# Kernel tuning notes

Hardware: AMD Instinct MI355X
Metric: run time of the kernel (lower is better)

Reference implementation:

```python
import jax, jax.numpy as jnp
import numpy as np
from jax import lax

B, T, D, H = 4, 2048, 1024, 8
DK = D // H        # head qk dim (expand_k=1.0) = 128
DV = 2 * D // H    # head v dim (expand_v=2.0) = 256
C = 64             # retention chunk size


def setup_inputs() -> dict:
    key = jax.random.key(0)
    ks = jax.random.split(key, 7)
    s = 0.02
    return {
        "x": jax.random.normal(ks[0], (B, T, D), jnp.float32),
        "Wq": jax.random.normal(ks[1], (D, H * DK), jnp.float32) * s,
        "Wk": jax.random.normal(ks[2], (D, H * DK), jnp.float32) * s,
        "Wv": jax.random.normal(ks[3], (D, H * DV), jnp.float32) * s,
        "Wg": jax.random.normal(ks[4], (D, H * DV), jnp.float32) * s,
        "Wo": jax.random.normal(ks[5], (H * DV, D), jnp.float32) * s,
        "norm_w": jnp.ones((DV,), jnp.float32),
    }


def _rope(x):
    # x: [B,T,H,DK]; GPT-NeoX style (non-interleaved) rotary, base 10000
    half = DK // 2
    inv = 1.0 / (10000.0 ** (jnp.arange(0, DK, 2, dtype=jnp.float32) / DK))
    f = jnp.arange(T, dtype=jnp.float32)[:, None] * inv[None, :]  # [T, half]
    cos = jnp.cos(f)[None, :, None, :]
    sin = jnp.sin(f)[None, :, None, :]
    x1, x2 = x[..., :half], x[..., half:]
    return jnp.concatenate([x1 * cos - x2 * sin, x2 * cos + x1 * sin], axis=-1)


def _retention(q, k, v):
    # chunked decay-gated linear attention (RetNet retention)
    # q,k: [B,T,H,DK], v: [B,T,H,DV]; recurrence S_t = g*S_{t-1} + k_t^T v_t, o_t = q_t S_t
    N = T // C
    gamma = 1.0 - 2.0 ** (-5.0 - jnp.arange(H, dtype=jnp.float32))  # [H] per-head decay
    i = jnp.arange(C, dtype=jnp.float32)
    expo = i[:, None] - i[None, :]                                   # [C,C]
    M = jnp.where(expo >= 0, gamma[:, None, None] ** expo[None], 0.0)  # [H,C,C] intra-chunk decay mask
    dec_q = gamma[:, None] ** (i + 1.0)        # [H,C] decay of state seen by q_i
    dec_k = gamma[:, None] ** (C - 1.0 - i)    # [H,C] decay of k_j into end-of-chunk state
    gC = gamma ** C

    def to_chunks(t):
        return t.reshape(B, N, C, H, -1).transpose(1, 0, 3, 2, 4)  # [N,B,H,C,d]

    qs, kcs, vcs = to_chunks(q), to_chunks(k), to_chunks(v)

    def step(S, inp):
        qc, kc, vc = inp  # [B,H,C,DK],[B,H,C,DK],[B,H,C,DV]
        attn = jnp.einsum('bhid,bhjd->bhij', qc, kc) * M[None]
        o_intra = jnp.einsum('bhij,bhje->bhie', attn, vc)
        o_inter = jnp.einsum('bhid,bhde->bhie', qc, S) * dec_q[None, :, :, None]
        kv = jnp.einsum('bhjd,bhje->bhde', kc * dec_k[None, :, :, None], vc)
        S_new = gC[None, :, None, None] * S + kv
        return S_new, o_intra + o_inter

    S0 = jnp.zeros((B, H, DK, DV), q.dtype)
    _, os_ = lax.scan(step, S0, (qs, kcs, vcs))  # os_: [N,B,H,C,DV]
    return os_.transpose(1, 0, 3, 2, 4).reshape(B, T, H, DV)


def reference(x, Wq, Wk, Wv, Wg, Wo, norm_w):
    q = (x @ Wq).reshape(B, T, H, DK)
    k = (x @ Wk).reshape(B, T, H, DK)
    v = (x @ Wv).reshape(B, T, H, DV)
    g = (x @ Wg).reshape(B, T, H, DV)
    q, k = _rope(q), _rope(k)
    q = q * (DK ** -0.5)
    o = _retention(q, k, v)
    # fused per-head RMSNorm + swish output gate (FusedRMSNormSwishGate)
    rms = jnp.sqrt(jnp.mean(o * o, axis=-1, keepdims=True) + 1e-5)
    o = (o / rms) * norm_w
    o = o * g * jax.nn.sigmoid(g)
    return o.reshape(B, T, H * DV) @ Wo
```

## Files before the change

kernel.cpp:

```cpp
#include <hip/hip_runtime.h>
#include <hip/hip_bf16.h>
#include <cstdint>
#include <cstddef>

using f32x4 = __attribute__((ext_vector_type(4))) float;
using s16x8 = __attribute__((ext_vector_type(8))) short;
using s16x4 = __attribute__((ext_vector_type(4))) short;

#define DEVINL __device__ __forceinline__

static constexpr int T_LEN  = 2048;
static constexpr int MROWS  = 8192;
static constexpr int NCHUNK = 32;

DEVINL float bf2f(short s){
  unsigned u = ((unsigned)(unsigned short)s) << 16;
  return __builtin_bit_cast(float, u);
}
DEVINL short f2bf(float f){
  unsigned u = __builtin_bit_cast(unsigned, f);
  u = (u + 0x7fffu + ((u >> 16) & 1u)) >> 16;
  return (short)(unsigned short)u;
}

#define GLOAD16(gp, lp) \
  __builtin_amdgcn_global_load_lds((__attribute__((address_space(1))) void*)(gp), \
                                   (__attribute__((address_space(3))) void*)(lp), 16, 0, 0)

#define MFMA16(a, b, c) __builtin_amdgcn_mfma_f32_16x16x32_bf16((a), (b), (c), 0, 0, 0)
#define SBAR()  __builtin_amdgcn_sched_barrier(0)
#define WAITLGKM(n) asm volatile("s_waitcnt lgkmcnt(" #n ")" ::: "memory")
#define WAITVM(n)   asm volatile("s_waitcnt vmcnt(" #n ")" ::: "memory")

__global__ __launch_bounds__(256) void cvt_f32_bf16(const float* __restrict__ in,
                                                    short* __restrict__ out, int n4){
  int i = blockIdx.x * 256 + threadIdx.x;
  if (i >= n4) return;
  float4 v = ((const float4*)in)[i];
  short4 o;
  o.x = f2bf(v.x); o.y = f2bf(v.y); o.z = f2bf(v.z); o.w = f2bf(v.w);
  ((short4*)out)[i] = o;
}

__global__ __launch_bounds__(256) void tr_w(const float* __restrict__ in,
                                            short* __restrict__ out, int R, int C){
  __shared__ float tile[32][33];
  int c0 = blockIdx.x * 32, r0 = blockIdx.y * 32;
  int tx = threadIdx.x, ty = threadIdx.y;
  #pragma unroll
  for (int i = 0; i < 4; ++i){
    int r = ty + i * 8;
    tile[r][tx] = in[(size_t)(r0 + r) * C + c0 + tx];
  }
  __syncthreads();
  #pragma unroll
  for (int i = 0; i < 4; ++i){
    int c = ty + i * 8;
    out[(size_t)(c0 + c) * R + r0 + tx] = f2bf(tile[tx][c]);
  }
}

__global__ __launch_bounds__(256) void tr_w4(const float* __restrict__ Wq,
                                             const float* __restrict__ Wk,
                                             const float* __restrict__ Wv,
                                             const float* __restrict__ Wg,
                                             short* __restrict__ WT){
  __shared__ float tile[32][33];
  int bx = blockIdx.x;
  const float* src; int C; size_t off; int cb;
  if (bx < 32)       { src = Wq; C = 1024; off = 0;                       cb = bx; }
  else if (bx < 64)  { src = Wk; C = 1024; off = (size_t)1024 * 1024;     cb = bx - 32; }
  else if (bx < 128) { src = Wg; C = 2048; off = (size_t)2048 * 1024;     cb = bx - 64; }
  else               { src = Wv; C = 2048; off = (size_t)4096 * 1024;     cb = bx - 128; }
  int c0 = cb * 32, r0 = blockIdx.y * 32;
  int tx = threadIdx.x, ty = threadIdx.y;
  #pragma unroll
  for (int i = 0; i < 4; ++i){
    int r = ty + i * 8;
    tile[r][tx] = src[(size_t)(r0 + r) * C + c0 + tx];
  }
  __syncthreads();
  #pragma unroll
  for (int i = 0; i < 4; ++i){
    int c = ty + i * 8;
    WT[off + (size_t)(c0 + c) * 1024 + r0 + tx] = f2bf(tile[tx][c]);
  }
}

__global__ __launch_bounds__(256) void tr_k_decay(const short* __restrict__ in,
                                                  short* __restrict__ out){
  __shared__ float tile[32][33];
  int c0 = blockIdx.x * 32, r0 = blockIdx.y * 32;
  int tx = threadIdx.x, ty = threadIdx.y;
  #pragma unroll
  for (int i = 0; i < 4; ++i){
    int r = ty + i * 8;
    tile[r][tx] = bf2f(in[(size_t)(r0 + r) * 1024 + c0 + tx]);
  }
  __syncthreads();
  #pragma unroll
  for (int i = 0; i < 4; ++i){
    int c  = c0 + ty + i * 8;
    int h  = c >> 7;
    float lg = log2f(1.0f - exp2f(-(float)(5 + h)));
    int srow = r0 + tx;
    int j = srow & 63;
    float dec = exp2f((float)(63 - j) * lg);
    out[(size_t)c * MROWS + srow] = f2bf(tile[tx][ty + i * 8] * dec);
  }
}

__global__ __launch_bounds__(256) void rope_table(float* __restrict__ tab){
  int i = blockIdx.x * 256 + threadIdx.x;
  int t = i >> 6, d = i & 63;
  float inv = exp2f(-(float)d * (13.287712379549449f / 64.0f));
  float f = (float)t * inv;
  float s, c;
  sincosf(f, &s, &c);
  tab[2 * i]     = c;
  tab[2 * i + 1] = s;
}

__global__ __launch_bounds__(256) void rope2(short* __restrict__ qb, short* __restrict__ kb,
                                             const float* __restrict__ tab){
  int idx = blockIdx.x * 256 + threadIdx.x;
  int bt  = idx >> 9, rem = idx & 511;
  int h   = rem >> 6, d = rem & 63;
  int t   = bt & (T_LEN - 1);
  float2 cs = ((const float2*)tab)[t * 64 + d];
  short* dst; float mult;
  if (blockIdx.y == 0){
    dst = qb;
    float lg = log2f(1.0f - exp2f(-(float)(5 + h)));
    mult = 0.08838834764831845f * exp2f((float)((t & 63) + 1) * lg);
  } else {
    dst = kb; mult = 1.0f;
  }
  size_t base = (size_t)bt * 1024 + h * 128 + d;
  float x1 = bf2f(dst[base]), x2 = bf2f(dst[base + 64]);
  dst[base]      = f2bf((x1 * cs.x - x2 * cs.y) * mult);
  dst[base + 64] = f2bf((x2 * cs.x + x1 * cs.y) * mult);
}

DEVINL s16x8 frag64(const short* buf, int row, int ks, int lhi){
  int ch = (ks * 4 + lhi) ^ (row & 7);
  return *(const s16x8*)&buf[row * 64 + ch * 8];
}

template<int MODE>
__global__ __launch_bounds__(512, 2) void gemm256(const short* __restrict__ A,
                                                  const short* __restrict__ Bt,
                                                  void* __restrict__ o0, void* __restrict__ o1,
                                                  void* __restrict__ o2, void* __restrict__ o3,
                                                  int K, int nt, int NT){
  constexpr int BM   = (MODE == 2 ? 128 : 256);
  constexpr int ABUF = BM * 64;
  constexpr int MF   = BM / 32;
  constexpr int RPP  = MF / 4;
  __shared__ alignas(16) short LBUF[3 * ABUF + 2 * 16384];
  short* const BB = LBUF + 3 * ABUF;
  const int tid = threadIdx.x, wave = tid >> 6, lane = tid & 63;
  const int l15 = lane & 15, lhi = lane >> 4;
  const int wm = (wave >> 2) * (BM / 2), wn = (wave & 3) * 64;
  const int MG  = (gridDim.x >> 3) / NT;
  const int xcd = blockIdx.x & 7, idx = blockIdx.x >> 3;
  const int mi  = idx % MG, nn = idx / MG;
  const int m0  = (xcd * MG + mi) * BM, n0 = nn * 256;
  const short* Ag = A + (size_t)m0 * K;
  const short* Bg = Bt + (size_t)n0 * K;
  const int sr = lane >> 3;
  const int gc = ((lane & 7) ^ sr) * 8;
  f32x4 acc[MF][4] = {};

  auto stageA = [&](int t, int half){
    short* lb = LBUF + (t % 3) * ABUF;
    size_t k0 = (size_t)t * 64;
    if constexpr (BM == 256){
      #pragma unroll
      for (int c = 0; c < 2; ++c){
        int r0 = half * 128 + c * 64;
        GLOAD16(Ag + (size_t)(r0 + wave * 8 + sr) * K + k0 + gc, lb + (r0 + wave * 8) * 64);
      }
    } else {
      int r0 = half * 64;
      GLOAD16(Ag + (size_t)(r0 + wave * 8 + sr) * K + k0 + gc, lb + (r0 + wave * 8) * 64);
    }
  };
  auto stageB = [&](int t, int half){
    short* lb = BB + (t & 1) * 16384;
    size_t k0 = (size_t)t * 64;
    #pragma unroll
    for (int c = 0; c < 2; ++c){
      int r0 = half * 128 + c * 64;
      GLOAD16(Bg + (size_t)(r0 + wave * 8 + sr) * K + k0 + gc, lb + (r0 + wave * 8) * 64);
    }
  };

  stageA(0, 0); stageA(0, 1); stageB(0, 0); stageB(0, 1);
  stageA(1, 0); stageA(1, 1); stageB(1, 0); stageB(1, 1);
  if constexpr (BM == 256) WAITVM(8); else WAITVM(6);
  SBAR();
  __builtin_amdgcn_s_barrier();

  for (int t = 0; t < nt; ++t){
    const short* Ab = LBUF + (t % 3) * ABUF;
    const short* Bb = BB + (t & 1) * 16384;
    s16x8 bfr[2][4];
    #pragma unroll
    for (int q = 0; q < 4; ++q){
      if (q == 0){
        #pragma unroll
        for (int ks = 0; ks < 2; ++ks)
          #pragma unroll
          for (int nf = 0; nf < 4; ++nf)
            bfr[ks][nf] = frag64(Bb, wn + nf * 16 + l15, ks, lhi);
      }
      s16x8 af[RPP][2];
      #pragma unroll
      for (int i = 0; i < RPP; ++i)
        #pragma unroll
        for (int ks = 0; ks < 2; ++ks)
          af[i][ks] = frag64(Ab, wm + (RPP * q + i) * 16 + l15, ks, lhi);
      if (t + 2 < nt){
        if (q == 0) stageA(t + 2, 0);
        if (q == 1) stageA(t + 2, 1);
        if (q == 2) stageB(t + 2, 0);
        if (q == 3) stageB(t + 2, 1);
      }
      SBAR();
      __builtin_amdgcn_s_barrier();
      WAITLGKM(0);
      SBAR();
      __builtin_amdgcn_s_setprio(1);
      #pragma unroll
      for (int i = 0; i < RPP; ++i)
        #pragma unroll
        for (int nf = 0; nf < 4; ++nf)
          #pragma unroll
          for (int ks = 0; ks < 2; ++ks){
            if constexpr (MODE == 4)
              acc[RPP * q + i][nf] = MFMA16(af[i][ks], bfr[ks][nf], acc[RPP * q + i][nf]);
            else
              acc[RPP * q + i][nf] = MFMA16(bfr[ks][nf], af[i][ks], acc[RPP * q + i][nf]);
          }
      __builtin_amdgcn_s_setprio(0);
      if (q == 3){
        if (t < nt - 2){
          if constexpr (BM == 256) WAITVM(8); else WAITVM(6);
        } else if (t == nt - 2){
          WAITVM(0);
        }
        SBAR();
      }
      __builtin_amdgcn_s_barrier();
    }
  }
  if constexpr (MODE == 2){
    float* dst = (float*)o0;
    #pragma unroll
    for (int mf = 0; mf < MF; ++mf){
      int m = m0 + wm + mf * 16 + l15;
      #pragma unroll
      for (int nf = 0; nf < 4; ++nf){
        int nb = n0 + wn + nf * 16 + 4 * lhi;
        *(float4*)&dst[(size_t)m * 1024 + nb] = *(float4*)&acc[mf][nf];
      }
    }
  } else if constexpr (MODE == 4){
    short* dst = (short*)o2;
    #pragma unroll
    for (int mf = 0; mf < MF; ++mf){
      int rb = m0 + wm + mf * 16 + 4 * lhi;
      #pragma unroll
      for (int nf = 0; nf < 4; ++nf){
        int e = n0 + wn + nf * 16 + l15;
        s16x4 pk;
        #pragma unroll
        for (int r = 0; r < 4; ++r) pk[r] = f2bf(acc[mf][nf][r]);
        *(s16x4*)&dst[(size_t)e * MROWS + rb] = pk;
      }
    }
  } else {
    short* dst; int ld, cb;
    if (n0 < 1024)      { dst = (short*)o0; ld = 1024; cb = n0; }
    else if (n0 < 2048) { dst = (short*)o1; ld = 1024; cb = n0 - 1024; }
    else                { dst = (short*)o3; ld = 2048; cb = n0 - 2048; }
    #pragma unroll
    for (int mf = 0; mf < MF; ++mf){
      int m = m0 + wm + mf * 16 + l15;
      #pragma unroll
      for (int nf = 0; nf < 4; ++nf){
        int nb = cb + wn + nf * 16 + 4 * lhi;
        s16x4 pk;
        #pragma unroll
        for (int r = 0; r < 4; ++r) pk[r] = f2bf(acc[mf][nf][r]);
        *(s16x4*)&dst[(size_t)m * ld + nb] = pk;
      }
    }
  }
}

__global__ __launch_bounds__(256) void ret_scan(const short* __restrict__ kT,
                                                const short* __restrict__ vT,
                                                short* __restrict__ ST){
  __shared__ alignas(16) short kbuf[3][4096];
  __shared__ alignas(16) short vbuf[3][4096];
  const int tid = threadIdx.x, wave = tid >> 6, lane = tid & 63;
  const int db = blockIdx.x & 1, eb = blockIdx.x >> 1;
  const int h = blockIdx.y, b = blockIdx.z;
  const int d0 = db * 64, e0 = eb * 64;
  const float lg = log2f(1.0f - exp2f(-(float)(5 + h)));
  const float gC = exp2f(64.0f * lg);
  f32x4 Sacc[4] = {};
  const int srow = wave * 8 + (lane >> 3);
  const int sc   = lane & 7;

  auto STAGE = [&](int n, int buf){
    size_t rowbase = (size_t)(b * T_LEN + n * 64);
    #pragma unroll
    for (int c = 0; c < 2; ++c){
      int r = c * 32 + srow;
      int gc2 = sc ^ (r & 7);
      GLOAD16(kT + (size_t)(h * 128 + d0 + r) * MROWS + rowbase + gc2 * 8,
              &kbuf[buf][c * 2048 + wave * 512]);
    }
    #pragma unroll
    for (int c = 0; c < 2; ++c){
      int r = c * 32 + srow;
      int gc2 = sc ^ (r & 7);
      GLOAD16(vT + (size_t)(h * 256 + e0 + r) * MROWS + rowbase + gc2 * 8,
              &vbuf[buf][c * 2048 + wave * 512]);
    }
  };

  STAGE(0, 0);
  STAGE(1, 1);
  for (int n = 0; n < NCHUNK; ++n){
    const int buf = n % 3;
    if (n + 2 < NCHUNK) STAGE(n + 2, (n + 2) % 3);
    if (n > 0){
      size_t stb = (((size_t)n * 4 + b) * 8 + h) * 32768;
      int dbase = d0 + 16 * wave + 4 * (lane >> 4);
      #pragma unroll
      for (int nf = 0; nf < 4; ++nf){
        int e = e0 + nf * 16 + (lane & 15);
        s16x4 pk;
        #pragma unroll
        for (int r = 0; r < 4; ++r) pk[r] = f2bf(Sacc[nf][r]);
        *(s16x4*)&ST[stb + (size_t)e * 128 + dbase] = pk;
      }
    }
    if (n == 0)       WAITVM(8);
    else if (n < 30)  WAITVM(12);
    else if (n == 30) WAITVM(8);
    else              WAITVM(4);
    __builtin_amdgcn_s_barrier();
    SBAR();
    #pragma unroll
    for (int nf = 0; nf < 4; ++nf)
      #pragma unroll
      for (int r = 0; r < 4; ++r) Sacc[nf][r] *= gC;
    #pragma unroll
    for (int ks = 0; ks < 2; ++ks){
      int d = 16 * wave + (lane & 15);
      int chA = (ks * 4 + (lane >> 4)) ^ (d & 7);
      s16x8 af = *(const s16x8*)&kbuf[buf][d * 64 + chA * 8];
      #pragma unroll
      for (int nf = 0; nf < 4; ++nf){
        int e = nf * 16 + (lane & 15);
        int chB = (ks * 4 + (lane >> 4)) ^ (e & 7);
        s16x8 bv = *(const s16x8*)&vbuf[buf][e * 64 + chB * 8];
        Sacc[nf] = MFMA16(af, bv, Sacc[nf]);
      }
    }
    __builtin_amdgcn_s_barrier();
    SBAR();
  }
}

__global__ __launch_bounds__(256, 2) void ret_fused(const short* __restrict__ q,
                                                    const short* __restrict__ k,
                                                    const short* __restrict__ vT,
                                                    const short* __restrict__ ST,
                                                    const short* __restrict__ g,
                                                    const float* __restrict__ nw,
                                                    short* __restrict__ y){
  __shared__ alignas(16) short GS[16384];
  __shared__ alignas(16) float SS[256];
  __shared__ alignas(16) short XS[16896];
  short* PS = XS;
  short* YT = XS;
  const int tid = threadIdx.x, wave = tid >> 6, lane = tid & 63;
  const int l15 = lane & 15, lhi = lane >> 4;
  const int n = blockIdx.x, h = blockIdx.y, b = blockIdx.z;
  const size_t rowbase = (size_t)(b * T_LEN + n * 64);
  {
    int row = wave * 2 + (lane >> 5), sc32 = lane & 31;
    #pragma unroll
    for (int c = 0; c < 8; ++c){
      int r = c * 8 + row;
      GLOAD16(g + (rowbase + r) * 2048 + h * 256 + sc32 * 8, &GS[c * 2048 + wave * 512]);
    }
  }
  s16x8 Qf[4][4];
  #pragma unroll
  for (int rf = 0; rf < 4; ++rf)
    #pragma unroll
    for (int ks = 0; ks < 4; ++ks)
      Qf[rf][ks] = *(const s16x8*)&q[(rowbase + rf * 16 + l15) * 1024 + h * 128 + ks * 32 + lhi * 8];
  s16x8 Kf[4];
  #pragma unroll
  for (int ks = 0; ks < 4; ++ks)
    Kf[ks] = *(const s16x8*)&k[(rowbase + wave * 16 + l15) * 1024 + h * 128 + ks * 32 + lhi * 8];
  f32x4 accP[4] = {};
  #pragma unroll
  for (int ks = 0; ks < 4; ++ks)
    #pragma unroll
    for (int nf = 0; nf < 4; ++nf)
      accP[nf] = MFMA16(Kf[ks], Qf[nf][ks], accP[nf]);
  const float lg = log2f(1.0f - exp2f(-(float)(5 + h)));
  {
    int jb = wave * 16 + 4 * lhi;
    float dj[4];
    #pragma unroll
    for (int r = 0; r < 4; ++r) dj[r] = exp2f(-(float)(jb + r + 1) * lg);
    #pragma unroll
    for (int nf = 0; nf < 4; ++nf){
      int i = nf * 16 + l15;
      s16x4 pk;
      #pragma unroll
      for (int r = 0; r < 4; ++r)
        pk[r] = f2bf((i >= jb + r) ? accP[nf][r] * dj[r] : 0.0f);
      *(s16x4*)&PS[i * 72 + jb] = pk;
    }
  }
  f32x4 acc[4][4] = {};
  if (n){
    size_t stb = (((size_t)n * 4 + b) * 8 + h) * 32768;
    #pragma unroll
    for (int ks = 0; ks < 4; ++ks){
      s16x8 Sf[4];
      #pragma unroll
      for (int nf = 0; nf < 4; ++nf){
        int e = wave * 64 + nf * 16 + l15;
        Sf[nf] = *(const s16x8*)&ST[stb + (size_t)e * 128 + ks * 32 + lhi * 8];
      }
      #pragma unroll
      for (int mf = 0; mf < 4; ++mf)
        #pragma unroll
        for (int nf = 0; nf < 4; ++nf)
          acc[mf][nf] = MFMA16(Qf[mf][ks], Sf[nf], acc[mf][nf]);
    }
  }
  s16x8 Vf[2][4];
  #pragma unroll
  for (int ks2 = 0; ks2 < 2; ++ks2)
    #pragma unroll
    for (int nf = 0; nf < 4; ++nf){
      int e = wave * 64 + nf * 16 + l15;
      Vf[ks2][nf] = *(const s16x8*)&vT[(size_t)(h * 256 + e) * MROWS + rowbase + ks2 * 32 + lhi * 8];
    }
  __syncthreads();
  #pragma unroll
  for (int ks2 = 0; ks2 < 2; ++ks2){
    s16x8 Pf[4];
    #pragma unroll
    for (int mf = 0; mf < 4; ++mf)
      Pf[mf] = *(const s16x8*)&PS[(mf * 16 + l15) * 72 + ks2 * 32 + lhi * 8];
    #pragma unroll
    for (int mf = 0; mf < 4; ++mf)
      #pragma unroll
      for (int nf = 0; nf < 4; ++nf)
        acc[mf][nf] = MFMA16(Pf[mf], Vf[ks2][nf], acc[mf][nf]);
  }
  float ssp[4][4];
  #pragma unroll
  for (int mf = 0; mf < 4; ++mf)
    #pragma unroll
    for (int r = 0; r < 4; ++r){
      float s = 0.f;
      #pragma unroll
      for (int nf = 0; nf < 4; ++nf) s += acc[mf][nf][r] * acc[mf][nf][r];
      #pragma unroll
      for (int off = 8; off >= 1; off >>= 1) s += __shfl_xor(s, off, 64);
      ssp[mf][r] = s;
    }
  if (l15 == 0){
    #pragma unroll
    for (int mf = 0; mf < 4; ++mf)
      #pragma unroll
      for (int r = 0; r < 4; ++r){
        int row = mf * 16 + 4 * lhi + r;
        SS[row * 4 + wave] = ssp[mf][r];
      }
  }
  __syncthreads();
  #pragma unroll
  for (int mf = 0; mf < 4; ++mf){
    float rr[4];
    #pragma unroll
    for (int r = 0; r < 4; ++r){
      int row = mf * 16 + 4 * lhi + r;
      f32x4 s4 = *(const f32x4*)&SS[row * 4];
      float tot = s4[0] + s4[1] + s4[2] + s4[3];
      rr[r] = __builtin_amdgcn_rsqf(tot * (1.0f / 256.0f) + 1e-5f);
    }
    #pragma unroll
    for (int nf = 0; nf < 4; ++nf){
      int e = wave * 64 + nf * 16 + l15;
      float nwe = nw[e];
      #pragma unroll
      for (int r = 0; r < 4; ++r){
        int row = mf * 16 + 4 * lhi + r;
        float gf = bf2f(GS[row * 256 + e]);
        float sig = __builtin_amdgcn_rcpf(1.0f + exp2f(gf * -1.4426950408889634f));
        YT[row * 264 + e] = f2bf(acc[mf][nf][r] * rr[r] * nwe * gf * sig);
      }
    }
  }
  __syncthreads();
  #pragma unroll
  for (int it = 0; it < 8; ++it){
    int flat = it * 2048 + tid * 8;
    int row = flat >> 8, e = flat & 255;
    s16x8 v = *(const s16x8*)&YT[row * 264 + e];
    *(s16x8*)&y[(rowbase + row) * 2048 + h * 256 + e] = v;
  }
}

extern "C" void kernel_launch(void* const* d_in, const int* in_sizes, int n_in,
                              void* d_out, int out_size, void* d_ws, size_t ws_size,
                              hipStream_t stream){
  const float* x  = (const float*)d_in[0];
  const float* Wq = (const float*)d_in[1];
  const float* Wk = (const float*)d_in[2];
  const float* Wv = (const float*)d_in[3];
  const float* Wg = (const float*)d_in[4];
  const float* Wo = (const float*)d_in[5];
  const float* nw = (const float*)d_in[6];
  float* out = (float*)d_out;

  char* w = (char*)d_ws;
  short* xb  = (short*)w;               w += (size_t)8192 * 1024 * 2;
  short* WT  = (short*)w;               w += (size_t)6144 * 1024 * 2;
  short* kTt = (short*)w;               w += (size_t)1024 * 8192 * 2;
  short* qb  = (short*)w;               w += (size_t)8192 * 1024 * 2;
  short* kb  = (short*)w;               w += (size_t)8192 * 1024 * 2;
  short* vT  = (short*)w;               w += (size_t)2048 * 8192 * 2;
  short* gb  = (short*)w;               w += (size_t)8192 * 2048 * 2;
  short* STb = (short*)w;               w += (size_t)32 * 4 * 8 * 32768 * 2;
  short* WoT = (short*)w;               w += (size_t)1024 * 2048 * 2;
  short* yb  = (short*)d_ws;
  float* tab = (float*)STb;

  cvt_f32_bf16<<<8192, 256, 0, stream>>>(x, xb, 8192 * 1024 / 4);
  dim3 tb(32, 8);
  tr_w4<<<dim3(192, 32), tb, 0, stream>>>(Wq, Wk, Wv, Wg, WT);
  tr_w <<<dim3(32, 64),  tb, 0, stream>>>(Wo, WoT, 2048, 1024);
  rope_table<<<512, 256, 0, stream>>>(tab);

  gemm256<3><<<512, 512, 0, stream>>>(xb, WT, qb, kb, nullptr, gb, 1024, 16, 16);
  gemm256<4><<<256, 512, 0, stream>>>(xb, WT + (size_t)4096 * 1024, nullptr, nullptr, vT, nullptr,
                                      1024, 16, 8);

  rope2<<<dim3(16384, 2), 256, 0, stream>>>(qb, kb, tab);
  tr_k_decay<<<dim3(32, 256), tb, 0, stream>>>(kb, kTt);

  ret_scan <<<dim3(8, 8, 4),  256, 0, stream>>>(kTt, vT, STb);
  ret_fused<<<dim3(32, 8, 4), 256, 0, stream>>>(qb, kb, vT, STb, gb, nw, yb);

  gemm256<2><<<256, 512, 0, stream>>>(yb, WoT, out, nullptr, nullptr, nullptr, 2048, 32, 4);
}
```

Before: 290.5 us.

## Software-pipeline LDS fragment reads against MFMAs in the bf16 GEMM main loop

Restructures the GEMM K-loop into a manually unrolled-by-two macro that prefetches the next quarter's A fragments, and the next tile's B fragments, into double-buffered registers. Partial lgkmcnt waits replace full waits, so LDS reads overlap the preceding MFMA group instead of stalling before each quarter. The aim is to hide LDS latency and cut barrier-induced bubbles, at the cost of more live registers. The loop now assumes an even tile count. The vmcnt wait is fixed at 8 for both tile heights, which may not match the load count issued when BM is 128.

Result: slower. 478.1 us (+64.6%).

```diff
diff --git a/kernel.cpp b/kernel.cpp
--- a/kernel.cpp
+++ b/kernel.cpp
@@ -29,8 +29,15 @@
 
 #define MFMA16(a, b, c) __builtin_amdgcn_mfma_f32_16x16x32_bf16((a), (b), (c), 0, 0, 0)
 #define SBAR()  __builtin_amdgcn_sched_barrier(0)
-#define WAITLGKM(n) asm volatile("s_waitcnt lgkmcnt(" #n ")" ::: "memory")
 #define WAITVM(n)   asm volatile("s_waitcnt vmcnt(" #n ")" ::: "memory")
+
+template<int N> DEVINL void wlgkm(){
+  if constexpr (N == 0)      asm volatile("s_waitcnt lgkmcnt(0)" ::: "memory");
+  else if constexpr (N == 2) asm volatile("s_waitcnt lgkmcnt(2)" ::: "memory");
+  else if constexpr (N == 4) asm volatile("s_waitcnt lgkmcnt(4)" ::: "memory");
+  else if constexpr (N == 6) asm volatile("s_waitcnt lgkmcnt(6)" ::: "memory");
+  else                       asm volatile("s_waitcnt lgkmcnt(8)" ::: "memory");
+}
 
 __global__ __launch_bounds__(256) void cvt_f32_bf16(const float* __restrict__ in,
                                                     short* __restrict__ out, int n4){
@@ -147,6 +154,19 @@
   return *(const s16x8*)&buf[row * 64 + ch * 8];
 }
 
+template<int MODE, int MFt, int RPPt, int Q, int KS>
+DEVINL void mfma_half(f32x4 (&acc)[MFt][4], s16x8 (&As)[RPPt][2], s16x8 (&Bs)[4]){
+  #pragma unroll
+  for (int i = 0; i < RPPt; ++i)
+    #pragma unroll
+    for (int nf = 0; nf < 4; ++nf){
+      if constexpr (MODE == 4)
+        acc[RPPt * Q + i][nf] = MFMA16(As[i][KS], Bs[nf], acc[RPPt * Q + i][nf]);
+      else
+        acc[RPPt * Q + i][nf] = MFMA16(Bs[nf], As[i][KS], acc[RPPt * Q + i][nf]);
+    }
+}
+
 template<int MODE>
 __global__ __launch_bounds__(512, 2) void gemm256(const short* __restrict__ A,
                                                   const short* __restrict__ Bt,
@@ -158,7 +178,7 @@
   constexpr int MF   = BM / 32;
   constexpr int RPP  = MF / 4;
   __shared__ alignas(16) short LBUF[3 * ABUF + 2 * 16384];
-  short* const BB = LBUF + 3 * ABUF;
+  short* const BBUF = LBUF + 3 * ABUF;
   const int tid = threadIdx.x, wave = tid >> 6, lane = tid & 63;
   const int l15 = lane & 15, lhi = lane >> 4;
   const int wm = (wave >> 2) * (BM / 2), wn = (wave & 3) * 64;
@@ -171,6 +191,8 @@
   const int sr = lane >> 3;
   const int gc = ((lane & 7) ^ sr) * 8;
   f32x4 acc[MF][4] = {};
+  s16x8 B0[4], B1[4], BC2[4];
+  s16x8 AA[RPP][2], AB2[RPP][2];
 
   auto stageA = [&](int t, int half){
     short* lb = LBUF + (t % 3) * ABUF;
@@ -187,7 +209,7 @@
     }
   };
   auto stageB = [&](int t, int half){
-    short* lb = BB + (t & 1) * 16384;
+    short* lb = BBUF + (t & 1) * 16384;
     size_t k0 = (size_t)t * 64;
     #pragma unroll
     for (int c = 0; c < 2; ++c){
@@ -195,66 +217,89 @@
       GLOAD16(Bg + (size_t)(r0 + wave * 8 + sr) * K + k0 + gc, lb + (r0 + wave * 8) * 64);
     }
   };
+  auto rdB = [&](s16x8 (&dst)[4], const short* Bb, int ks){
+    #pragma unroll
+    for (int nf = 0; nf < 4; ++nf) dst[nf] = frag64(Bb, wn + nf * 16 + l15, ks, lhi);
+  };
+  auto rdA = [&](s16x8 (&dst)[RPP][2], const short* Ab, int q){
+    #pragma unroll
+    for (int i = 0; i < RPP; ++i)
+      #pragma unroll
+      for (int ks = 0; ks < 2; ++ks)
+        dst[i][ks] = frag64(Ab, wm + (RPP * q + i) * 16 + l15, ks, lhi);
+  };
+
+#define GTILE(T, BK0, BNX)                                                        \
+  {                                                                               \
+    const int t_ = (T);                                                           \
+    const short* Ab  = LBUF + (t_ % 3) * ABUF;                                    \
+    const short* Anb = LBUF + ((t_ + 1) % 3) * ABUF;                              \
+    const short* Bb  = BBUF + (t_ & 1) * 16384;                                   \
+    const short* Bnb = BBUF + ((t_ + 1) & 1) * 16384;                             \
+       \
+    __builtin_amdgcn_s_barrier();                                                 \
+    if (t_ + 2 < nt) stageA(t_ + 2, 0);                                           \
+    rdB(BC2, Bb, 1); SBAR();                                                      \
+    rdA(AB2, Ab, 1); SBAR();                                                      \
+    wlgkm<4 + 2 * RPP>(); SBAR();                                                 \
+    __builtin_amdgcn_s_setprio(1);                                                \
+    mfma_half<MODE, MF, RPP, 0, 0>(acc, AA, BK0);                                 \
+    __builtin_amdgcn_s_setprio(0);                                                \
+    wlgkm<2 * RPP>(); SBAR();                                                     \
+    __builtin_amdgcn_s_setprio(1);                                                \
+    mfma_half<MODE, MF, RPP, 0, 1>(acc, AA, BC2);                                 \
+    __builtin_amdgcn_s_setprio(0);                                                \
+                                                                     \
+    __builtin_amdgcn_s_barrier();                                                 \
+    if (t_ + 2 < nt) stageA(t_ + 2, 1);                                           \
+    rdA(AA, Ab, 2); SBAR();                                                       \
+    wlgkm<2 * RPP>(); SBAR();                                                     \
+    __builtin_amdgcn_s_setprio(1);                                                \
+    mfma_half<MODE, MF, RPP, 1, 0>(acc, AB2, BK0);                                \
+    mfma_half<MODE, MF, RPP, 1, 1>(acc, AB2, BC2);                                \
+    __builtin_amdgcn_s_setprio(0);                                                \
+                                                                     \
+    __builtin_amdgcn_s_barrier();                                                 \
+    if (t_ + 2 < nt) stageB(t_ + 2, 0);                                           \
+    rdA(AB2, Ab, 3); SBAR();                                                      \
+    wlgkm<2 * RPP>(); SBAR();                                                     \
+    __builtin_amdgcn_s_setprio(1);                                                \
+    mfma_half<MODE, MF, RPP, 2, 0>(acc, AA, BK0);                                 \
+    mfma_half<MODE, MF, RPP, 2, 1>(acc, AA, BC2);                                 \
+    __builtin_amdgcn_s_setprio(0);                                                \
+    \
+    __builtin_amdgcn_s_barrier();                                                 \
+    if (t_ + 2 < nt) stageB(t_ + 2, 1);                                           \
+    if (t_ + 1 < nt){                                                             \
+      if (t_ == nt - 2){ WAITVM(0); } else { WAITVM(8); }                         \
+      SBAR();                                                                     \
+      __builtin_amdgcn_s_barrier();                                               \
+      rdB(BNX, Bnb, 0); SBAR();                                                   \
+      rdA(AA, Anb, 0); SBAR();                                                    \
+      wlgkm<4 + 2 * RPP>(); SBAR();                                               \
+    } else {                                                                      \
+      wlgkm<0>(); SBAR();                                                         \
+    }                                                                             \
+    __builtin_amdgcn_s_setprio(1);                                                \
+    mfma_half<MODE, MF, RPP, 3, 0>(acc, AB2, BK0);                                \
+    mfma_half<MODE, MF, RPP, 3, 1>(acc, AB2, BC2);                                \
+    __builtin_amdgcn_s_setprio(0);                                                \
+  }
 
   stageA(0, 0); stageA(0, 1); stageB(0, 0); stageB(0, 1);
   stageA(1, 0); stageA(1, 1); stageB(1, 0); stageB(1, 1);
-  if constexpr (BM == 256) WAITVM(8); else WAITVM(6);
+  WAITVM(8);
   SBAR();
   __builtin_amdgcn_s_barrier();
-
-  for (int t = 0; t < nt; ++t){
-    const short* Ab = LBUF + (t % 3) * ABUF;
-    const short* Bb = BB + (t & 1) * 16384;
-    s16x8 bfr[2][4];
-    #pragma unroll
-    for (int q = 0; q < 4; ++q){
-      if (q == 0){
-        #pragma unroll
-        for (int ks = 0; ks < 2; ++ks)
-          #pragma unroll
-          for (int nf = 0; nf < 4; ++nf)
-            bfr[ks][nf] = frag64(Bb, wn + nf * 16 + l15, ks, lhi);
-      }
-      s16x8 af[RPP][2];
-      #pragma unroll
-      for (int i = 0; i < RPP; ++i)
-        #pragma unroll
-        for (int ks = 0; ks < 2; ++ks)
-          af[i][ks] = frag64(Ab, wm + (RPP * q + i) * 16 + l15, ks, lhi);
-      if (t + 2 < nt){
-        if (q == 0) stageA(t + 2, 0);
-        if (q == 1) stageA(t + 2, 1);
-        if (q == 2) stageB(t + 2, 0);
-        if (q == 3) stageB(t + 2, 1);
-      }
-      SBAR();
-      __builtin_amdgcn_s_barrier();
-      WAITLGKM(0);
-      SBAR();
-      __builtin_amdgcn_s_setprio(1);
-      #pragma unroll
-      for (int i = 0; i < RPP; ++i)
-        #pragma unroll
-        for (int nf = 0; nf < 4; ++nf)
-          #pragma unroll
-          for (int ks = 0; ks < 2; ++ks){
-            if constexpr (MODE == 4)
-              acc[RPP * q + i][nf] = MFMA16(af[i][ks], bfr[ks][nf], acc[RPP * q + i][nf]);
-            else
-              acc[RPP * q + i][nf] = MFMA16(bfr[ks][nf], af[i][ks], acc[RPP * q + i][nf]);
-          }
-      __builtin_amdgcn_s_setprio(0);
-      if (q == 3){
-        if (t < nt - 2){
-          if constexpr (BM == 256) WAITVM(8); else WAITVM(6);
-        } else if (t == nt - 2){
-          WAITVM(0);
-        }
-        SBAR();
-      }
-      __builtin_amdgcn_s_barrier();
-    }
-  }
+  rdB(B0, BBUF, 0); SBAR();
+  rdA(AA, LBUF, 0); SBAR();
+
+  for (int tt = 0; tt < nt; tt += 2){
+    GTILE(tt,     B0, B1);
+    GTILE(tt + 1, B1, B0);
+  }
+#undef GTILE
+
   if constexpr (MODE == 2){
     float* dst = (float*)o0;
     #pragma unroll
```

## Split output GEMM over K with 256-row tiles and add partials

Applied to the files above, without the earlier changes.

The output projection GEMM now uses 256-row tiles instead of 128 and splits its K=2048 reduction into two halves across blockIdx.y. Each half writes an fp32 partial into workspace, and a separate add2 kernel sums the two partials into the output. The MFMA loop order is also changed to iterate ks outermost. The goal is more reuse per tile while keeping the same number of blocks. The cost is writing and re-reading 64 MB of fp32 partials plus one extra kernel launch.

Result: slower. 304.7 us (+4.9%).

```diff
diff --git a/kernel.cpp b/kernel.cpp
--- a/kernel.cpp
+++ b/kernel.cpp
@@ -40,6 +40,17 @@
   short4 o;
   o.x = f2bf(v.x); o.y = f2bf(v.y); o.z = f2bf(v.z); o.w = f2bf(v.w);
   ((short4*)out)[i] = o;
+}
+
+__global__ __launch_bounds__(256) void add2(const float* __restrict__ a,
+                                            const float* __restrict__ b,
+                                            float* __restrict__ o, int n4){
+  int i = blockIdx.x * 256 + threadIdx.x;
+  if (i >= n4) return;
+  float4 x = ((const float4*)a)[i];
+  float4 y = ((const float4*)b)[i];
+  x.x += y.x; x.y += y.y; x.z += y.z; x.w += y.w;
+  ((float4*)o)[i] = x;
 }
 
 __global__ __launch_bounds__(256) void tr_w(const float* __restrict__ in,
@@ -153,7 +164,7 @@
                                                   void* __restrict__ o0, void* __restrict__ o1,
                                                   void* __restrict__ o2, void* __restrict__ o3,
                                                   int K, int nt, int NT){
-  constexpr int BM   = (MODE == 2 ? 128 : 256);
+  constexpr int BM   = 256;
   constexpr int ABUF = BM * 64;
   constexpr int MF   = BM / 32;
   constexpr int RPP  = MF / 4;
@@ -166,8 +177,10 @@
   const int xcd = blockIdx.x & 7, idx = blockIdx.x >> 3;
   const int mi  = idx % MG, nn = idx / MG;
   const int m0  = (xcd * MG + mi) * BM, n0 = nn * 256;
-  const short* Ag = A + (size_t)m0 * K;
-  const short* Bg = Bt + (size_t)n0 * K;
+  size_t koff = 0;
+  if constexpr (MODE == 2) koff = (size_t)blockIdx.y * 1024;
+  const short* Ag = A + (size_t)m0 * K + koff;
+  const short* Bg = Bt + (size_t)n0 * K + koff;
   const int sr = lane >> 3;
   const int gc = ((lane & 7) ^ sr) * 8;
   f32x4 acc[MF][4] = {};
@@ -175,14 +188,9 @@
   auto stageA = [&](int t, int half){
     short* lb = LBUF + (t % 3) * ABUF;
     size_t k0 = (size_t)t * 64;
-    if constexpr (BM == 256){
-      #pragma unroll
-      for (int c = 0; c < 2; ++c){
-        int r0 = half * 128 + c * 64;
-        GLOAD16(Ag + (size_t)(r0 + wave * 8 + sr) * K + k0 + gc, lb + (r0 + wave * 8) * 64);
-      }
-    } else {
-      int r0 = half * 64;
+    #pragma unroll
+    for (int c = 0; c < 2; ++c){
+      int r0 = half * 128 + c * 64;
       GLOAD16(Ag + (size_t)(r0 + wave * 8 + sr) * K + k0 + gc, lb + (r0 + wave * 8) * 64);
     }
   };
@@ -198,7 +206,7 @@
 
   stageA(0, 0); stageA(0, 1); stageB(0, 0); stageB(0, 1);
   stageA(1, 0); stageA(1, 1); stageB(1, 0); stageB(1, 1);
-  if constexpr (BM == 256) WAITVM(8); else WAITVM(6);
+  WAITVM(8);
   SBAR();
   __builtin_amdgcn_s_barrier();
 
@@ -233,11 +241,11 @@
       SBAR();
       __builtin_amdgcn_s_setprio(1);
       #pragma unroll
-      for (int i = 0; i < RPP; ++i)
-        #pragma unroll
-        for (int nf = 0; nf < 4; ++nf)
+      for (int ks = 0; ks < 2; ++ks)
+        #pragma unroll
+        for (int i = 0; i < RPP; ++i)
           #pragma unroll
-          for (int ks = 0; ks < 2; ++ks){
+          for (int nf = 0; nf < 4; ++nf){
             if constexpr (MODE == 4)
               acc[RPP * q + i][nf] = MFMA16(af[i][ks], bfr[ks][nf], acc[RPP * q + i][nf]);
             else
@@ -245,18 +253,15 @@
           }
       __builtin_amdgcn_s_setprio(0);
       if (q == 3){
-        if (t < nt - 2){
-          if constexpr (BM == 256) WAITVM(8); else WAITVM(6);
-        } else if (t == nt - 2){
-          WAITVM(0);
-        }
+        if (t < nt - 2)       { WAITVM(8); }
+        else if (t == nt - 2) { WAITVM(0); }
         SBAR();
       }
       __builtin_amdgcn_s_barrier();
     }
   }
   if constexpr (MODE == 2){
-    float* dst = (float*)o0;
+    float* dst = (float*)o0 + (size_t)blockIdx.y * 8192 * 1024;
     #pragma unroll
     for (int mf = 0; mf < MF; ++mf){
       int m = m0 + wm + mf * 16 + l15;
@@ -552,6 +557,7 @@
   short* WoT = (short*)w;               w += (size_t)1024 * 2048 * 2;
   short* yb  = (short*)d_ws;
   float* tab = (float*)STb;
+  float* Pp  = (float*)STb;
 
   cvt_f32_bf16<<<8192, 256, 0, stream>>>(x, xb, 8192 * 1024 / 4);
   dim3 tb(32, 8);
@@ -569,5 +575,6 @@
   ret_scan <<<dim3(8, 8, 4),  256, 0, stream>>>(kTt, vT, STb);
   ret_fused<<<dim3(32, 8, 4), 256, 0, stream>>>(qb, kb, vT, STb, gb, nw, yb);
 
-  gemm256<2><<<256, 512, 0, stream>>>(yb, WoT, out, nullptr, nullptr, nullptr, 2048, 32, 4);
-}
+  gemm256<2><<<dim3(128, 2), 512, 0, stream>>>(yb, WoT, Pp, nullptr, nullptr, nullptr, 2048, 16, 4);
+  add2<<<8192, 256, 0, stream>>>(Pp, Pp + (size_t)8192 * 1024, out, 8192 * 1024 / 4);
+}
```

## Restructure GEMM main loop into two halves with fewer barriers

Applied to the files above, without the earlier changes.

Replaces the four-quarter inner loop, which had a barrier and an explicit lgkmcnt wait per quarter, with two halves. Each half loads half of the A fragments and runs its MFMAs, and there are only two barriers per k-tile. The A prefetch is issued in the first half and the B prefetch after the mid barrier. The manual sched_barriers and lgkmcnt waits are removed, leaving LDS wait placement to the compiler. The intent is to cut synchronization overhead and raise MFMA density, at the cost of more live fragment registers and less explicit control over instruction scheduling.

After: 282.2 us. 1.03x faster.

```diff
diff --git a/kernel.cpp b/kernel.cpp
--- a/kernel.cpp
+++ b/kernel.cpp
@@ -29,7 +29,6 @@
 
 #define MFMA16(a, b, c) __builtin_amdgcn_mfma_f32_16x16x32_bf16((a), (b), (c), 0, 0, 0)
 #define SBAR()  __builtin_amdgcn_sched_barrier(0)
-#define WAITLGKM(n) asm volatile("s_waitcnt lgkmcnt(" #n ")" ::: "memory")
 #define WAITVM(n)   asm volatile("s_waitcnt vmcnt(" #n ")" ::: "memory")
 
 __global__ __launch_bounds__(256) void cvt_f32_bf16(const float* __restrict__ in,
@@ -156,7 +155,7 @@
   constexpr int BM   = (MODE == 2 ? 128 : 256);
   constexpr int ABUF = BM * 64;
   constexpr int MF   = BM / 32;
-  constexpr int RPP  = MF / 4;
+  constexpr int MH   = MF / 2;
   __shared__ alignas(16) short LBUF[3 * ABUF + 2 * 16384];
   short* const BB = LBUF + 3 * ABUF;
   const int tid = threadIdx.x, wave = tid >> 6, lane = tid & 63;
@@ -199,61 +198,63 @@
   stageA(0, 0); stageA(0, 1); stageB(0, 0); stageB(0, 1);
   stageA(1, 0); stageA(1, 1); stageB(1, 0); stageB(1, 1);
   if constexpr (BM == 256) WAITVM(8); else WAITVM(6);
-  SBAR();
   __builtin_amdgcn_s_barrier();
 
   for (int t = 0; t < nt; ++t){
     const short* Ab = LBUF + (t % 3) * ABUF;
     const short* Bb = BB + (t & 1) * 16384;
     s16x8 bfr[2][4];
-    #pragma unroll
-    for (int q = 0; q < 4; ++q){
-      if (q == 0){
+    s16x8 af[MH][2];
+    #pragma unroll
+    for (int ks = 0; ks < 2; ++ks)
+      #pragma unroll
+      for (int nf = 0; nf < 4; ++nf)
+        bfr[ks][nf] = frag64(Bb, wn + nf * 16 + l15, ks, lhi);
+    #pragma unroll
+    for (int i = 0; i < MH; ++i)
+      #pragma unroll
+      for (int ks = 0; ks < 2; ++ks)
+        af[i][ks] = frag64(Ab, wm + i * 16 + l15, ks, lhi);
+    if (t + 2 < nt){ stageA(t + 2, 0); stageA(t + 2, 1); }
+    __builtin_amdgcn_s_setprio(1);
+    #pragma unroll
+    for (int ks = 0; ks < 2; ++ks)
+      #pragma unroll
+      for (int i = 0; i < MH; ++i)
         #pragma unroll
-        for (int ks = 0; ks < 2; ++ks)
-          #pragma unroll
-          for (int nf = 0; nf < 4; ++nf)
-            bfr[ks][nf] = frag64(Bb, wn + nf * 16 + l15, ks, lhi);
-      }
-      s16x8 af[RPP][2];
-      #pragma unroll
-      for (int i = 0; i < RPP; ++i)
+        for (int nf = 0; nf < 4; ++nf){
+          if constexpr (MODE == 4)
+            acc[i][nf] = MFMA16(af[i][ks], bfr[ks][nf], acc[i][nf]);
+          else
+            acc[i][nf] = MFMA16(bfr[ks][nf], af[i][ks], acc[i][nf]);
+        }
+    __builtin_amdgcn_s_setprio(0);
+    __builtin_amdgcn_s_barrier();
+    if (t + 2 < nt){ stageB(t + 2, 0); stageB(t + 2, 1); }
+    #pragma unroll
+    for (int i = 0; i < MH; ++i)
+      #pragma unroll
+      for (int ks = 0; ks < 2; ++ks)
+        af[i][ks] = frag64(Ab, wm + (MH + i) * 16 + l15, ks, lhi);
+    __builtin_amdgcn_s_setprio(1);
+    #pragma unroll
+    for (int ks = 0; ks < 2; ++ks)
+      #pragma unroll
+      for (int i = 0; i < MH; ++i)
         #pragma unroll
-        for (int ks = 0; ks < 2; ++ks)
-          af[i][ks] = frag64(Ab, wm + (RPP * q + i) * 16 + l15, ks, lhi);
-      if (t + 2 < nt){
-        if (q == 0) stageA(t + 2, 0);
-        if (q == 1) stageA(t + 2, 1);
-        if (q == 2) stageB(t + 2, 0);
-        if (q == 3) stageB(t + 2, 1);
-      }
-      SBAR();
-      __builtin_amdgcn_s_barrier();
-      WAITLGKM(0);
-      SBAR();
-      __builtin_amdgcn_s_setprio(1);
-      #pragma unroll
-      for (int i = 0; i < RPP; ++i)
-        #pragma unroll
-        for (int nf = 0; nf < 4; ++nf)
-          #pragma unroll
-          for (int ks = 0; ks < 2; ++ks){
-            if constexpr (MODE == 4)
-              acc[RPP * q + i][nf] = MFMA16(af[i][ks], bfr[ks][nf], acc[RPP * q + i][nf]);
-            else
-              acc[RPP * q + i][nf] = MFMA16(bfr[ks][nf], af[i][ks], acc[RPP * q + i][nf]);
-          }
-      __builtin_amdgcn_s_setprio(0);
-      if (q == 3){
-        if (t < nt - 2){
-          if constexpr (BM == 256) WAITVM(8); else WAITVM(6);
-        } else if (t == nt - 2){
-          WAITVM(0);
+        for (int nf = 0; nf < 4; ++nf){
+          if constexpr (MODE == 4)
+            acc[MH + i][nf] = MFMA16(af[i][ks], bfr[ks][nf], acc[MH + i][nf]);
+          else
+            acc[MH + i][nf] = MFMA16(bfr[ks][nf], af[i][ks], acc[MH + i][nf]);
         }
-        SBAR();
-      }
-      __builtin_amdgcn_s_barrier();
-    }
+    __builtin_amdgcn_s_setprio(0);
+    if (t < nt - 2){
+      if constexpr (BM == 256) WAITVM(8); else WAITVM(6);
+    } else if (t == nt - 2){
+      WAITVM(0);
+    }
+    __builtin_amdgcn_s_barrier();
   }
   if constexpr (MODE == 2){
     float* dst = (float*)o0;
```
